# Kernel tuning notes

Measured on AMD Instinct MI355X. Metric: run time of the kernel, lower is better.

The kernel has to match this reference:

```python
import jax, jax.numpy as jnp
import numpy as np

N, F_IN, Z, H, E, ATT, NPER, B = 4096, 512, 256, 256, 64, 128, 16, 128

def setup_inputs() -> dict:
    key = jax.random.key(0)
    ks = jax.random.split(key, 30)
    nrm = lambda k, s, sc=0.05: jax.random.normal(k, s, dtype=jnp.float32) * sc
    return {
        "comm_adj0": jax.random.uniform(ks[0], (N, N), dtype=jnp.float32),
        "comm_adj1": jax.random.uniform(ks[1], (N, N), dtype=jnp.float32),
        "diff_adj0": jax.random.uniform(ks[2], (N, N), dtype=jnp.float32),
        "diff_adj1": jax.random.uniform(ks[3], (N, N), dtype=jnp.float32),
        "feats": nrm(ks[4], (N, F_IN), 1.0),
        "W_comm_gnn": nrm(ks[5], (F_IN, H)), "b_comm_gnn": jnp.zeros((H,), jnp.float32),
        "W_diff_gnn": nrm(ks[6], (F_IN, H)), "b_diff_gnn": jnp.zeros((H,), jnp.float32),
        "W_catt1": nrm(ks[7], (H, ATT)), "b_catt1": jnp.zeros((ATT,), jnp.float32), "w_catt2": nrm(ks[8], (ATT, 1)),
        "W_datt1": nrm(ks[9], (H, ATT)), "b_datt1": jnp.zeros((ATT,), jnp.float32), "w_datt2": nrm(ks[10], (ATT, 1)),
        "W_mu_c": nrm(ks[11], (H, E)), "b_mu_c": jnp.zeros((E,), jnp.float32),
        "W_var_c": nrm(ks[12], (H, E)), "b_var_c": jnp.zeros((E,), jnp.float32),
        "W_mu_d": nrm(ks[13], (H, E)), "b_mu_d": jnp.zeros((E,), jnp.float32),
        "W_var_d": nrm(ks[14], (H, E)), "b_var_d": jnp.zeros((E,), jnp.float32),
        "W_z1_gc1": nrm(ks[15], (F_IN, Z)), "b_z1_gc1": jnp.zeros((Z,), jnp.float32),
        "W_z1_gc2": nrm(ks[16], (Z, Z)), "b_z1_gc2": jnp.zeros((Z,), jnp.float32),
        "wb_z1": jax.random.uniform(ks[17], (2, 1), dtype=jnp.float32, maxval=0.1),
        "Wt_comm": nrm(ks[18], (NPER, E)), "Wt_diff": nrm(ks[19], (NPER, E)),
        "W_z2_gc1": nrm(ks[20], (F_IN, Z)), "b_z2_gc1": jnp.zeros((Z,), jnp.float32),
        "W_z2_gc2": nrm(ks[21], (Z, Z)), "b_z2_gc2": jnp.zeros((Z,), jnp.float32),
        "wb_z2": jax.random.uniform(ks[22], (2, 1), dtype=jnp.float32, maxval=0.1),
        "xs": jax.random.randint(ks[23], (B,), 0, N),
    }

def _gcn(x, adj, W, b):
    # DenseGCNConv: set diag to 1 (self loops), sym-normalize with deg clamped to >=1
    n = adj.shape[0]
    eye = jnp.eye(n, dtype=adj.dtype)
    adj = adj * (1.0 - eye) + eye
    d = jnp.maximum(jnp.sum(adj, axis=-1), 1.0) ** -0.5
    adj_n = d[:, None] * adj * d[None, :]
    return adj_n @ (x @ W) + b

def _attention(z, W1, b1, w2):
    # z: [N, K, H] -> [N, H]
    w = jnp.tanh(z @ W1 + b1) @ w2              # [N, K, 1]
    beta = jax.nn.softmax(jnp.mean(w, axis=0), axis=0)  # [K, 1]
    return jnp.sum(beta[None] * z, axis=1)

def _adj_gen(ctx, Wt):
    # ctx: [N, E], Wt: [P, E]; mean over P of cosine-sim maps, then relu-mask
    cf = ctx[None, :, :] * Wt[:, None, :]                     # [P, N, E]
    cn = cf / jnp.maximum(jnp.linalg.norm(cf, axis=-1, keepdims=True), 1e-12)
    att = jnp.einsum('pne,pme->nm', cn, cn) / Wt.shape[0]     # mean over P without [P,N,N]
    return jnp.maximum(att, 0.0)

def reference(comm_adj0, comm_adj1, diff_adj0, diff_adj1, feats,
              W_comm_gnn, b_comm_gnn, W_diff_gnn, b_diff_gnn,
              W_catt1, b_catt1, w_catt2, W_datt1, b_datt1, w_datt2,
              W_mu_c, b_mu_c, W_var_c, b_var_c, W_mu_d, b_mu_d, W_var_d, b_var_d,
              W_z1_gc1, b_z1_gc1, W_z1_gc2, b_z1_gc2, wb_z1,
              Wt_comm, Wt_diff, W_z2_gc1, b_z2_gc1, W_z2_gc2, b_z2_gc2, wb_z2, xs):
    relu = jax.nn.relu
    comm_adjs = [comm_adj0, comm_adj1]
    diff_adjs = [diff_adj0, diff_adj1]
    # --- q_e2_gs_e1 (eval: dropout=id, reparameterize -> mu) ---
    comm_reps = [relu(_gcn(feats, a, W_comm_gnn, b_comm_gnn)) for a in comm_adjs]
    comm_adj_mean = (comm_adj0 + comm_adj1) * 0.5
    diff_reps = [relu(_gcn(feats, a + comm_adj_mean, W_diff_gnn, b_diff_gnn)) for a in diff_adjs]
    comm_agg = _attention(jnp.stack(comm_reps, axis=1), W_catt1, b_catt1, w_catt2)
    diff_agg = _attention(jnp.stack(comm_reps + diff_reps, axis=1), W_datt1, b_datt1, w_datt2)
    mu_c = relu(comm_agg @ W_mu_c + b_mu_c)
    var_c = jax.nn.sigmoid(relu(comm_agg @ W_var_c + b_var_c))
    mu_d = relu(diff_agg @ W_mu_d + b_mu_d)
    var_d = jax.nn.sigmoid(relu(diff_agg @ W_var_d + b_var_d))
    comm_samples, diff_samples = mu_c, mu_d
    # --- p_z1_gs_e1 (mean pooling over adj stacks) ---
    diff_adj_mean = (diff_adj0 + diff_adj1) * 0.5
    tmp = comm_adj_mean * wb_z1[0, 0] + diff_adj_mean * wb_z1[1, 0]
    final_A1 = tmp + tmp.T
    U1 = relu(_gcn(feats, final_A1, W_z1_gc1, b_z1_gc1))
    U2 = relu(_gcn(U1, final_A1, W_z1_gc2, b_z1_gc2))
    z1 = (U1 + U2) * 0.5
    # --- p_z2_e2 ---
    ca = _adj_gen(comm_samples, Wt_comm)
    da = _adj_gen(diff_samples, Wt_diff)
    tmp2 = ca * wb_z2[0, 0] + da * wb_z2[1, 0]
    final_A2 = tmp2 + tmp2.T
    V1 = relu(_gcn(feats, final_A2, W_z2_gc1, b_z2_gc1))
    V2 = relu(_gcn(V1, final_A2, W_z2_gc2, b_z2_gc2))
    z2 = (V1 + V2) * 0.5
    h = jnp.concatenate([z1, z2], axis=1)
    return (h[xs], mu_c, var_c, mu_d, var_d)
```

## Files before the change

kernel.cpp:

```cpp
#include <hip/hip_runtime.h>
#include <math.h>

using f32x4 = __attribute__((ext_vector_type(4))) float;
using bf16x8 = __attribute__((ext_vector_type(8))) short;
#define MFMA16 __builtin_amdgcn_mfma_f32_16x16x32_bf16
static constexpr size_t M1c = 1048576;

__device__ __forceinline__ float wave_reduce_sum(float v) {
#pragma unroll
  for (int off = 32; off > 0; off >>= 1) v += __shfl_down(v, off);
  return v;
}

__device__ __forceinline__ unsigned short f2bf_rne(float x) {
  unsigned int u = __float_as_uint(x);
  unsigned int r = u + 0x7FFFu + ((u >> 16) & 1u);
  return (unsigned short)(r >> 16);
}
__device__ __forceinline__ void split1(float x, unsigned short& h, unsigned short& l) {
  unsigned int u = __float_as_uint(x);
  h = (unsigned short)(u >> 16);
  float rem = x - __uint_as_float(u & 0xFFFF0000u);
  l = f2bf_rne(rem);
}
// ... 59 lines not shown
  int r0 = blockIdx.y * 128;
  const float4* T4 = (const float4*)T;
  float4 a = make_float4(0.f, 0.f, 0.f, 0.f);
  for (int r = r0; r < r0 + 128; ++r) {
    float4 p = T4[(size_t)r * 1024 + c4];
    a.x += p.x; a.y += p.y; a.z += p.z; a.w += p.w;
  }
  atomicAdd(&cs[c4 * 4 + 0], a.x);
  atomicAdd(&cs[c4 * 4 + 1], a.y);
  atomicAdd(&cs[c4 * 4 + 2], a.z);
  atomicAdd(&cs[c4 * 4 + 3], a.w);
}

__global__ __launch_bounds__(256) void k_addTn(const float* __restrict__ T,
                                               const float* __restrict__ dv,
                                               unsigned short* __restrict__ A1h,
                                               unsigned short* __restrict__ A1l) {
  __shared__ float t[64][65];
  int bi = blockIdx.y, bj = blockIdx.x;
  int r = threadIdx.x >> 4;
  int c4 = threadIdx.x & 15;
#pragma unroll
  for (int rr = 0; rr < 4; ++rr) {
    int row = rr * 16 + r;
    float4 v = *(const float4*)(T + (size_t)(bj * 64 + row) * 4096 + bi * 64 + c4 * 4);
    t[row][c4 * 4 + 0] = v.x; t[row][c4 * 4 + 1] = v.y;
    t[row][c4 * 4 + 2] = v.z; t[row][c4 * 4 + 3] = v.w;
  }
  __syncthreads();
#pragma unroll
  for (int rr = 0; rr < 4; ++rr) {
    int ro = rr * 16 + r;
    int rowg = bi * 64 + ro;
    float dr = dv[rowg];
    size_t idx = (size_t)rowg * 4096 + bj * 64 + c4 * 4;
    float4 a = *(const float4*)(T + idx);
    float f0 = (a.x + t[c4 * 4 + 0][ro]) * dr * dv[bj * 64 + c4 * 4 + 0];
    float f1 = (a.y + t[c4 * 4 + 1][ro]) * dr * dv[bj * 64 + c4 * 4 + 1];
    float f2 = (a.z + t[c4 * 4 + 2][ro]) * dr * dv[bj * 64 + c4 * 4 + 2];
    float f3 = (a.w + t[c4 * 4 + 3][ro]) * dr * dv[bj * 64 + c4 * 4 + 3];
    ushort4 hv, lv;
    split1(f0, ((unsigned short*)&hv)[0], ((unsigned short*)&lv)[0]);
    split1(f1, ((unsigned short*)&hv)[1], ((unsigned short*)&lv)[1]);
    split1(f2, ((unsigned short*)&hv)[2], ((unsigned short*)&lv)[2]);
    split1(f3, ((unsigned short*)&hv)[3], ((unsigned short*)&lv)[3]);
    *(ushort4*)(A1h + idx) = hv;
    *(ushort4*)(A1l + idx) = lv;
  }
}

__global__ __launch_bounds__(256) void k_fin(
    const float* __restrict__ rs_c0, const float* __restrict__ rs_c1,
    const float* __restrict__ rs_d0, const float* __restrict__ rs_d1,
    const float* __restrict__ dg_c0, const float* __restrict__ dg_c1,
    const float* __restrict__ dg_d0, const float* __restrict__ dg_d1,
    const float* __restrict__ cs_tmp, const float* __restrict__ wb,
    float* __restrict__ d_c0, float* __restrict__ d_c1,
    float* __restrict__ d_dd0, float* __restrict__ d_dd1, float* __restrict__ d_A1,
    float* __restrict__ gP_dd0, float* __restrict__ gP_dd1, float* __restrict__ gP_A1) {
  int n = blockIdx.x * 256 + threadIdx.x;
  float rc0 = rs_c0[n], rc1 = rs_c1[n], rd0 = rs_d0[n], rd1 = rs_d1[n];
  float gc0 = dg_c0[n], gc1 = dg_c1[n], gd0 = dg_d0[n], gd1 = dg_d1[n];
  d_c0[n] = rsqrtf(fmaxf(rc0 - gc0 + 1.f, 1.f));
  d_c1[n] = rsqrtf(fmaxf(rc1 - gc1 + 1.f, 1.f));
  float cmr = 0.5f * (rc0 + rc1), cmg = 0.5f * (gc0 + gc1);
  float g0 = gd0 + cmg; gP_dd0[n] = g0;
  d_dd0[n] = rsqrtf(fmaxf(rd0 + cmr - g0 + 1.f, 1.f));
  float g1 = gd1 + cmg; gP_dd1[n] = g1;
  d_dd1[n] = rsqrtf(fmaxf(rd1 + cmr - g1 + 1.f, 1.f));
  float w0 = wb[0], w1 = wb[1];
  float rt = w0 * cmr + w1 * 0.5f * (rd0 + rd1);
  float gt = w0 * cmg + w1 * 0.5f * (gd0 + gd1);
  gP_A1[n] = 2.f * gt;
  d_A1[n] = rsqrtf(fmaxf(rt + cs_tmp[n] - 2.f * gt + 1.f, 1.f));
}

__global__ __launch_bounds__(256) void k_dA2(const float* __restrict__ rs,
                                             const float* __restrict__ gP,
                                             float* __restrict__ dvec) {
  int n = blockIdx.x * 256 + threadIdx.x;
  dvec[n] = rsqrtf(fmaxf(rs[n] - gP[n] + 1.f, 1.f));
}

__global__ __launch_bounds__(256) void k_cn(const float* __restrict__ mu,
                                            const float* __restrict__ Wt,
                                            unsigned short* __restrict__ Chh,
                                            unsigned short* __restrict__ Cll) {
  int g = blockIdx.x * 4 + (threadIdx.x >> 6);
  int lane = threadIdx.x & 63;
  int n = g >> 4, p = g & 15;
  float v = mu[(size_t)n * 64 + lane] * Wt[p * 64 + lane];
  float ss = v * v;
#pragma unroll
  for (int off = 32; off > 0; off >>= 1) ss += __shfl_xor(ss, off);
  float nrm = fmaxf(sqrtf(ss), 1e-12f);
  float r = v / nrm;
  unsigned short h, l;
  split1(r, h, l);
  size_t o = (size_t)n * 1024 + p * 64 + lane;
  Chh[o] = h; Cll[o] = l;
}

__global__ __launch_bounds__(256) void k_prepB(const float* __restrict__ X,
                                               const float* __restrict__ scale,
                                               unsigned short* __restrict__ Bh,
                                               unsigned short* __restrict__ Bl,
                                               int K, int C) {
  __shared__ float t[64][65];
  int kb = blockIdx.x * 64, cb = blockIdx.y * 64;
  int lane = threadIdx.x & 63, w = threadIdx.x >> 6;
  for (int i = 0; i < 16; ++i) {
    int kk = w * 16 + i;
    float s = scale ? scale[kb + kk] : 1.f;
    t[kk][lane] = X[(size_t)(kb + kk) * C + cb + lane] * s;
  }
  __syncthreads();
  for (int i = 0; i < 16; ++i) {
    int cc = w * 16 + i;
    float v = t[lane][cc];
    unsigned short h, l;
    split1(v, h, l);
    size_t o = (size_t)(cb + cc) * K + kb + lane;
    Bh[o] = h; Bl[o] = l;
  }
}

__global__ __launch_bounds__(256) void k_prop4S(
    const float* __restrict__ As0, const float* __restrict__ As1,
    const float* __restrict__ As2, const float* __restrict__ As3,
    const float* __restrict__ Ax0, const float* __restrict__ Ax1, int cmask,
    const float* __restrict__ dsc0, const float* __restrict__ dsc1,
    const float* __restrict__ dsc2, const float* __restrict__ dsc3,
    const unsigned short* __restrict__ B0h, const unsigned short* __restrict__ B0l,
    const unsigned short* __restrict__ B1h, const unsigned short* __restrict__ B1l,
    const unsigned short* __restrict__ B2h, const unsigned short* __restrict__ B2l,
    const unsigned short* __restrict__ B3h, const unsigned short* __restrict__ B3l,
    float* __restrict__ part, int K, int Kc, int KS) {
  int d = blockIdx.x;
  int q = gridDim.x >> 3;
  int lin = (d & 7) * q + (d >> 3);
  int mblk = lin & 63;
  int sk = lin >> 6;
  int seg = sk / KS, kb = sk % KS;
  const float* A = seg == 0 ? As0 : seg == 1 ? As1 : seg == 2 ? As2 : As3;
  const unsigned short* Bh = seg == 0 ? B0h : seg == 1 ? B1h : seg == 2 ? B2h : B3h;
  const unsigned short* Bl = seg == 0 ? B0l : seg == 1 ? B1l : seg == 2 ? B2l : B3l;
  const float* dsc = seg == 0 ? dsc0 : seg == 1 ? dsc1 : seg == 2 ? dsc2 : dsc3;
  const bool usecm = (cmask >> seg) & 1;
  const bool usesc = dsc != nullptr;
  __shared__ unsigned char sm[2][2][8192];
  const int tid = threadIdx.x;
  const int m0 = mblk * 64, k0 = kb * Kc;
  const int w = tid >> 6, lane = tid & 63;
  const int lr = lane & 15, lk = (lane >> 4) * 8, n0w = w * 64;
  const int srow = tid >> 2, skp = (tid & 3) * 8;
  const int swz = (srow & 7) << 4;
  const int offh = (srow * 128 + skp * 2) ^ swz;
  const int offl = (srow * 128 + 64 + skp * 2) ^ swz;
  const size_t rowoff = (size_t)(m0 + srow) * K + k0 + skp;
  const float* arow = A + rowoff;
  const float* xrow0 = Ax0 + rowoff;
  const float* xrow1 = Ax1 + rowoff;
  const float* scrow = usesc ? (dsc + k0 + skp) : nullptr;

  float4 xa0, xa1, xb0, xb1;
  float4 ya0, ya1, yb0, yb1;
  float4 za0, za1, zb0, zb1;
  float4 sa0, sa1, sb0, sb1;
  auto ldPair = [&](int kk) {
    xa0 = *(const float4*)(arow + kk);
    xa1 = *(const float4*)(arow + kk + 4);
    xb0 = *(const float4*)(arow + kk + 32);
    xb1 = *(const float4*)(arow + kk + 36);
    if (usecm) {
      ya0 = *(const float4*)(xrow0 + kk);
      ya1 = *(const float4*)(xrow0 + kk + 4);
      yb0 = *(const float4*)(xrow0 + kk + 32);
      yb1 = *(const float4*)(xrow0 + kk + 36);
      za0 = *(const float4*)(xrow1 + kk);
      za1 = *(const float4*)(xrow1 + kk + 4);
      zb0 = *(const float4*)(xrow1 + kk + 32);
      zb1 = *(const float4*)(xrow1 + kk + 36);
    }
// ... 32 lines not shown
      }
      if (usesc) {
        f[0] *= sb0.x; f[1] *= sb0.y; f[2] *= sb0.z; f[3] *= sb0.w;
        f[4] *= sb1.x; f[5] *= sb1.y; f[6] *= sb1.z; f[7] *= sb1.w;
      }
      bf16x8 hh, ll;
      split8(f, hh, ll);
      *(bf16x8*)(&sm[pb][1][0] + offh) = hh;
      *(bf16x8*)(&sm[pb][1][0] + offl) = ll;
    }
  };

  f32x4 acc[4][4] = {};
  auto comp = [&](int pb, int half, int kkg) {
    const unsigned char* base = &sm[pb][half][0];
    bf16x8 ah[4], al[4];
#pragma unroll
    for (int i = 0; i < 4; ++i) {
      int row = i * 16 + lr, sz = (row & 7) << 4;
      ah[i] = *(const bf16x8*)(base + ((row * 128 + lk * 2) ^ sz));
      al[i] = *(const bf16x8*)(base + ((row * 128 + 64 + lk * 2) ^ sz));
    }
#pragma unroll
    for (int j = 0; j < 4; ++j) {
      int col = n0w + j * 16 + lr;
      size_t bo = (size_t)col * K + kkg;
      bf16x8 bh = *(const bf16x8*)(Bh + bo);
      bf16x8 bl = *(const bf16x8*)(Bl + bo);
#pragma unroll
      for (int i = 0; i < 4; ++i) {
        acc[i][j] = MFMA16(ah[i], bh, acc[i][j], 0, 0, 0);
        acc[i][j] = MFMA16(ah[i], bl, acc[i][j], 0, 0, 0);
        acc[i][j] = MFMA16(al[i], bh, acc[i][j], 0, 0, 0);
      }
    }
  };

  int pairs = Kc / 64;
  ldPair(0);
  wrPair(0);
  __syncthreads();
  for (int p = 0; p < pairs; ++p) {
    if (p + 1 < pairs) ldPair((p + 1) * 64);
    comp(p & 1, 0, k0 + p * 64 + lk);
    comp(p & 1, 1, k0 + p * 64 + 32 + lk);
    if (p + 1 < pairs) wrPair((p + 1) & 1);
    __syncthreads();
  }
  int rr = (lane >> 4) * 4;
  float* Cp = part + (size_t)(seg * KS + kb) * M1c;
#pragma unroll
  for (int i = 0; i < 4; ++i)
#pragma unroll
    for (int j = 0; j < 4; ++j) {
      int col = n0w + j * 16 + lr;
#pragma unroll
      for (int r = 0; r < 4; ++r)
        Cp[(size_t)(m0 + i * 16 + rr + r) * 256 + col] = acc[i][j][r];
    }
}

__global__ __launch_bounds__(256) void k_gemmS(
    const unsigned short* __restrict__ Ah, const unsigned short* __restrict__ Al,
    const unsigned short* __restrict__ Bth, const unsigned short* __restrict__ Btl,
    float* __restrict__ part, int K, int Kc) {
  int d = blockIdx.x;
  int q = gridDim.x >> 3;
  int lin = (d & 7) * q + (d >> 3);
  int mblk = lin & 63;
  int kb = lin >> 6;
  __shared__ unsigned char sm[2][2][8192];
  const int tid = threadIdx.x;
  const int m0 = mblk * 64, k0 = kb * Kc;
  const int w = tid >> 6, lane = tid & 63;
  const int lr = lane & 15, lk = (lane >> 4) * 8, n0w = w * 64;
  const int srow = tid >> 2, skp = (tid & 3) * 8;
  const int swz = (srow & 7) << 4;
  const int offh = (srow * 128 + skp * 2) ^ swz;
  const int offl = (srow * 128 + 64 + skp * 2) ^ swz;
  const unsigned short* arh = Ah + (size_t)(m0 + srow) * K + k0 + skp;
  const unsigned short* arl = Al + (size_t)(m0 + srow) * K + k0 + skp;

  bf16x8 rha, rla, rhb, rlb;
  auto ldPair = [&](int kk) {
    rha = *(const bf16x8*)(arh + kk);
    rla = *(const bf16x8*)(arl + kk);
    rhb = *(const bf16x8*)(arh + kk + 32);
    rlb = *(const bf16x8*)(arl + kk + 32);
  };
  auto wrPair = [&](int pb) {
    *(bf16x8*)(&sm[pb][0][0] + offh) = rha;
    *(bf16x8*)(&sm[pb][0][0] + offl) = rla;
    *(bf16x8*)(&sm[pb][1][0] + offh) = rhb;
    *(bf16x8*)(&sm[pb][1][0] + offl) = rlb;
  };

  f32x4 acc[4][4] = {};
  auto comp = [&](int pb, int half, int kkg) {
    const unsigned char* base = &sm[pb][half][0];
    bf16x8 ah[4], al[4];
#pragma unroll
    for (int i = 0; i < 4; ++i) {
      int row = i * 16 + lr, sz = (row & 7) << 4;
      ah[i] = *(const bf16x8*)(base + ((row * 128 + lk * 2) ^ sz));
      al[i] = *(const bf16x8*)(base + ((row * 128 + 64 + lk * 2) ^ sz));
    }
#pragma unroll
    for (int j = 0; j < 4; ++j) {
      int col = n0w + j * 16 + lr;
      size_t bo = (size_t)col * K + kkg;
      bf16x8 bh = *(const bf16x8*)(Bth + bo);
      bf16x8 bl = *(const bf16x8*)(Btl + bo);
#pragma unroll
      for (int i = 0; i < 4; ++i) {
        acc[i][j] = MFMA16(ah[i], bh, acc[i][j], 0, 0, 0);
        acc[i][j] = MFMA16(ah[i], bl, acc[i][j], 0, 0, 0);
        acc[i][j] = MFMA16(al[i], bh, acc[i][j], 0, 0, 0);
      }
    }
  };

  int pairs = Kc / 64;
  ldPair(0);
  wrPair(0);
  __syncthreads();
  for (int p = 0; p < pairs; ++p) {
    if (p + 1 < pairs) ldPair((p + 1) * 64);
    comp(p & 1, 0, k0 + p * 64 + lk);
    comp(p & 1, 1, k0 + p * 64 + 32 + lk);
    if (p + 1 < pairs) wrPair((p + 1) & 1);
    __syncthreads();
  }
  int rr = (lane >> 4) * 4;
  float* Cp = part + (size_t)kb * M1c;
#pragma unroll
  for (int i = 0; i < 4; ++i)
#pragma unroll
    for (int j = 0; j < 4; ++j) {
      int col = n0w + j * 16 + lr;
#pragma unroll
      for (int r = 0; r < 4; ++r)
        Cp[(size_t)(m0 + i * 16 + rr + r) * 256 + col] = acc[i][j][r];
    }
}

__global__ __launch_bounds__(256) void k_gemmH(
    const float* __restrict__ Aa, const float* __restrict__ Ab,
    const unsigned short* __restrict__ Bth, const unsigned short* __restrict__ Btl,
    float* __restrict__ part, int K, int Kc) {
  __shared__ unsigned char sm[2][2][8192];
  const int tid = threadIdx.x;
  const int m0 = blockIdx.y * 64, k0 = blockIdx.x * Kc;
  const int w = tid >> 6, lane = tid & 63;
  const int lr = lane & 15, lk = (lane >> 4) * 8, n0w = w * 64;
  const int srow = tid >> 2, skp = (tid & 3) * 8;
  const int swz = (srow & 7) << 4;
  const int offh = (srow * 128 + skp * 2) ^ swz;
  const int offl = (srow * 128 + 64 + skp * 2) ^ swz;
  const int slot = w >> 1;

  auto stage = [&](int b, int kk) {
    int kg = k0 + kk + skp;
    const float* p = Aa + (size_t)(m0 + srow) * K + kg;
    float4 x0 = *(const float4*)(p), x1 = *(const float4*)(p + 4);
    float f[8] = {x0.x, x0.y, x0.z, x0.w, x1.x, x1.y, x1.z, x1.w};
    bf16x8 hh, ll;
    split8(f, hh, ll);
    *(bf16x8*)(&sm[b][0][0] + offh) = hh;
    *(bf16x8*)(&sm[b][0][0] + offl) = ll;
    const float* qq = Ab + (size_t)(m0 + srow) * K + kg;
    float4 y0 = *(const float4*)(qq), y1 = *(const float4*)(qq + 4);
    float g[8] = {y0.x, y0.y, y0.z, y0.w, y1.x, y1.y, y1.z, y1.w};
    split8(g, hh, ll);
    *(bf16x8*)(&sm[b][1][0] + offh) = hh;
    *(bf16x8*)(&sm[b][1][0] + offl) = ll;
  };

  f32x4 acc[4][4] = {};
  stage(0, 0);
  __syncthreads();
  int steps = Kc / 32;
  for (int s = 0; s < steps; ++s) {
    if (s + 1 < steps) stage((s + 1) & 1, (s + 1) * 32);
    const unsigned char* base = &sm[s & 1][slot][0];
    bf16x8 ah[4], al[4];
#pragma unroll
    for (int i = 0; i < 4; ++i) {
      int row = i * 16 + lr, sz = (row & 7) << 4;
      ah[i] = *(const bf16x8*)(base + ((row * 128 + lk * 2) ^ sz));
      al[i] = *(const bf16x8*)(base + ((row * 128 + 64 + lk * 2) ^ sz));
    }
    int kkg = k0 + s * 32 + lk;
#pragma unroll
    for (int j = 0; j < 4; ++j) {
      int col = n0w + j * 16 + lr;
      size_t bo = (size_t)col * K + kkg;
      bf16x8 bh = *(const bf16x8*)(Bth + bo);
      bf16x8 bl = *(const bf16x8*)(Btl + bo);
#pragma unroll
      for (int i = 0; i < 4; ++i) {
        acc[i][j] = MFMA16(ah[i], bh, acc[i][j], 0, 0, 0);
        acc[i][j] = MFMA16(ah[i], bl, acc[i][j], 0, 0, 0);
        acc[i][j] = MFMA16(al[i], bh, acc[i][j], 0, 0, 0);
      }
    }
    __syncthreads();
  }
  int rr = (lane >> 4) * 4;
  float* Cp = part + (size_t)blockIdx.x * M1c;
#pragma unroll
  for (int i = 0; i < 4; ++i)
#pragma unroll
    for (int j = 0; j < 4; ++j) {
// ... 146 lines not shown
        int sz = (rowb & 7) << 4;
        bf16x8 bh = *(const bf16x8*)(bb + ((rowb * 128 + lk * 2) ^ sz));
        bf16x8 bl = *(const bf16x8*)(bb + ((rowb * 128 + 64 + lk * 2) ^ sz));
#pragma unroll
        for (int i = 0; i < 4; ++i) {
          acc[i][j] = MFMA16(ah[i], bh, acc[i][j], 0, 0, 0);
          acc[i][j] = MFMA16(ah[i], bl, acc[i][j], 0, 0, 0);
          acc[i][j] = MFMA16(al[i], bh, acc[i][j], 0, 0, 0);
        }
      }
      if (s + 1 < 32) {
        wrT((s + 1) & 1, 0, rA);
        wrT((s + 1) & 1, 1, rB);
      }
      __syncthreads();
    }
  };

  f32x4 aC[4][4] = {}, aD[4][4] = {};
  gram(Ch, Cl, aC);
  gram(Dh, Dl, aD);

  float w0 = wb[0] * 0.125f, w1 = wb[1] * 0.125f;
  int rr = (lane >> 4) * 4;
  bool diag = (bi == bj);
#pragma unroll
  for (int i = 0; i < 4; ++i) {
#pragma unroll
    for (int r = 0; r < 4; ++r) {
      int row = rbase + wm * 64 + i * 16 + rr + r;
      float p = 0.f;
#pragma unroll
      for (int j = 0; j < 4; ++j) {
        int col = cbase + wn * 64 + j * 16 + lr;
        float v = w0 * fmaxf(aC[i][j][r], 0.f) + w1 * fmaxf(aD[i][j][r], 0.f);
        p += v;
        unsigned short h, l;
        split1(v, h, l);
        size_t o = (size_t)row * 4096 + col;
        A2h[o] = h; A2l[o] = l;
        if (diag && row == col) gP[row] = v;
      }
      p += __shfl_xor(p, 1); p += __shfl_xor(p, 2);
      p += __shfl_xor(p, 4); p += __shfl_xor(p, 8);
      if (lr == 0) atomicAdd(&rs[row], p);
    }
  }
  if (!diag) {
#pragma unroll
    for (int j = 0; j < 4; ++j) {
      int col = cbase + wn * 64 + j * 16 + lr;
      float cs = 0.f;
#pragma unroll
      for (int i = 0; i < 4; ++i) {
        int row0m = rbase + wm * 64 + i * 16 + rr;
        ushort4 hv, lv;
#pragma unroll
        for (int r = 0; r < 4; ++r) {
          float v = w0 * fmaxf(aC[i][j][r], 0.f) + w1 * fmaxf(aD[i][j][r], 0.f);
          cs += v;
          unsigned short h, l;
          split1(v, h, l);
          ((unsigned short*)&hv)[r] = h;
          ((unsigned short*)&lv)[r] = l;
        }
        *(ushort4*)(A2h + (size_t)col * 4096 + row0m) = hv;
        *(ushort4*)(A2l + (size_t)col * 4096 + row0m) = lv;
      }
      cs += __shfl_xor(cs, 16); cs += __shfl_xor(cs, 32);
      if (lane < 16) atomicAdd(&rs[col], cs);
    }
  }
}

__global__ __launch_bounds__(256) void k_redxw(
    const float* __restrict__ part, float* __restrict__ o0, float* __restrict__ o1,
    float* __restrict__ o2, float* __restrict__ o3) {
  int idx = blockIdx.x * 256 + threadIdx.x;
  size_t i4 = (size_t)idx * 4;
  int seg = (int)(i4 >> 20);
  size_t local = i4 & (M1c - 1);
  float4 a = make_float4(0.f, 0.f, 0.f, 0.f);
#pragma unroll
  for (int kb = 0; kb < 4; ++kb) {
    float4 p = *(const float4*)(part + (size_t)(seg * 4 + kb) * M1c + local);
    a.x += p.x; a.y += p.y; a.z += p.z; a.w += p.w;
  }
  float* o = seg == 0 ? o0 : seg == 1 ? o1 : seg == 2 ? o2 : o3;
  *(float4*)(o + local) = a;
}

__global__ __launch_bounds__(256) void k_ep_prop4(
    const float* __restrict__ part, const float* __restrict__ xwc,
    const float* __restrict__ xwd, const float* __restrict__ dv0,
    const float* __restrict__ dv1, const float* __restrict__ dv2,
    const float* __restrict__ dv3, const float* __restrict__ dg0,
    const float* __restrict__ dg1, const float* __restrict__ dg2,
    const float* __restrict__ dg3, const float* __restrict__ bc,
    const float* __restrict__ bd, float* __restrict__ o0, float* __restrict__ o1,
    float* __restrict__ o2, float* __restrict__ o3) {
  int idx = blockIdx.x * 256 + threadIdx.x;
  size_t i4 = (size_t)idx * 4;
  int seg = (int)(i4 >> 20);
  size_t local = i4 & (M1c - 1);
  int row = (int)(local >> 8), c = (int)(local & 255);
  float4 a = make_float4(0.f, 0.f, 0.f, 0.f);
#pragma unroll
  for (int kb = 0; kb < 2; ++kb) {
    float4 p = *(const float4*)(part + (size_t)(seg * 2 + kb) * M1c + local);
    a.x += p.x; a.y += p.y; a.z += p.z; a.w += p.w;
  }
  const float* xw = (seg < 2) ? xwc : xwd;
  const float* dvec = seg == 0 ? dv0 : seg == 1 ? dv1 : seg == 2 ? dv2 : dv3;
  const float* dgp = seg == 0 ? dg0 : seg == 1 ? dg1 : seg == 2 ? dg2 : dg3;
  const float* bias = (seg < 2) ? bc : bd;
  float* out = seg == 0 ? o0 : seg == 1 ? o1 : seg == 2 ? o2 : o3;
  float4 x = *(const float4*)(xw + local);
  float4 b = *(const float4*)(bias + c);
  float dn = dvec[row], dfix = (1.f - dgp[row]) * dn * dn;
  float4 o;
  o.x = fmaxf(dn * a.x + dfix * x.x + b.x, 0.f);
  o.y = fmaxf(dn * a.y + dfix * x.y + b.y, 0.f);
  o.z = fmaxf(dn * a.z + dfix * x.z + b.z, 0.f);
  o.w = fmaxf(dn * a.w + dfix * x.w + b.w, 0.f);
  *(float4*)(out + local) = o;
}

template <int PRENORM, int SPLITOUT>
__global__ __launch_bounds__(256) void k_ep_prop(
    const float* __restrict__ part, const float* __restrict__ xw,
    const float* __restrict__ dvec, const float* __restrict__ diag,
    const float* __restrict__ bias, float* __restrict__ out,
    unsigned short* __restrict__ oh, unsigned short* __restrict__ ol) {
  int idx = blockIdx.x * 256 + threadIdx.x;
  size_t i = (size_t)idx * 4;
  int row = (int)(i >> 8), c = (int)(i & 255);
  float4 a = make_float4(0.f, 0.f, 0.f, 0.f);
#pragma unroll
  for (int kb = 0; kb < 8; ++kb) {
    float4 p = *(const float4*)(part + (size_t)kb * M1c + i);
    a.x += p.x; a.y += p.y; a.z += p.z; a.w += p.w;
  }
  float4 x = *(const float4*)(xw + i);
  float4 b = *(const float4*)(bias + c);
  float dn = dvec[row], dfix = (1.f - diag[row]) * dn * dn;
  float s = PRENORM ? 1.f : dn;
  float4 o;
  o.x = fmaxf(s * a.x + dfix * x.x + b.x, 0.f);
  o.y = fmaxf(s * a.y + dfix * x.y + b.y, 0.f);
  o.z = fmaxf(s * a.z + dfix * x.z + b.z, 0.f);
  o.w = fmaxf(s * a.w + dfix * x.w + b.w, 0.f);
  *(float4*)(out + i) = o;
  if constexpr (SPLITOUT) {
    ushort4 hv, lv;
    split1(o.x, ((unsigned short*)&hv)[0], ((unsigned short*)&lv)[0]);
    split1(o.y, ((unsigned short*)&hv)[1], ((unsigned short*)&lv)[1]);
    split1(o.z, ((unsigned short*)&hv)[2], ((unsigned short*)&lv)[2]);
    split1(o.w, ((unsigned short*)&hv)[3], ((unsigned short*)&lv)[3]);
    *(ushort4*)(oh + i) = hv;
    *(ushort4*)(ol + i) = lv;
  }
}

__global__ __launch_bounds__(256) void k_red2(const float* __restrict__ part,
                                              float* __restrict__ out) {
  int idx = blockIdx.x * 256 + threadIdx.x;
  size_t i = (size_t)idx * 4;
  float4 p0 = *(const float4*)(part + i);
// ... 110 lines not shown
  const float* b_z1_2 = (const float*)d_in[26];
  const float* wb_z1 = (const float*)d_in[27];
  const float* Wt_c = (const float*)d_in[28];
  const float* Wt_d = (const float*)d_in[29];
  const float* W_z2_1 = (const float*)d_in[30];
  const float* b_z2_1 = (const float*)d_in[31];
  const float* W_z2_2 = (const float*)d_in[32];
  const float* b_z2_2 = (const float*)d_in[33];
  const float* wb_z2 = (const float*)d_in[34];
  const int* xs = (const int*)d_in[35];

  float* out = (float*)d_out;
  float* out_muc = out + 65536;
  float* out_varc = out + 327680;
  float* out_mud = out + 589824;
  float* out_vard = out + 851968;

  float* ws = (float*)d_ws;
  const size_t M1 = M1c;
  float* xw_comm = ws + 0 * M1;
  float* xw_diff = ws + 1 * M1;
  float* xw_z1 = ws + 2 * M1;
  float* xw_z2 = ws + 3 * M1;
  float* cr0 = ws + 4 * M1;
  float* cr1 = ws + 5 * M1;
  float* dr0 = ws + 6 * M1;
  float* dr1 = ws + 7 * M1;
  float* u1 = ws + 8 * M1;
  float* u2 = ws + 9 * M1;
  float* v1 = ws + 10 * M1;
  float* v2 = ws + 11 * M1;
  float* uw = ws + 12 * M1;
  float* cagg = ws + 13 * M1;
  float* dagg = ws + 14 * M1;
  float* accb4 = ws + 15 * M1;
  unsigned short* B4h[4];
  unsigned short* B4l[4];
  for (int t = 0; t < 4; ++t) {
    B4h[t] = (unsigned short*)(ws + (19 + t) * M1);
    B4l[t] = B4h[t] + (size_t)256 * 4096;
  }
  unsigned short* A1h = (unsigned short*)(ws + 23 * M1);
  unsigned short* A1l = (unsigned short*)(ws + 31 * M1);
  unsigned short* Cch = (unsigned short*)(ws + 23 * M1);
  unsigned short* Ccl = (unsigned short*)(ws + 25 * M1);
  unsigned short* Cdh = (unsigned short*)(ws + 27 * M1);
  unsigned short* Cdl = (unsigned short*)(ws + 29 * M1);
  float* partZ2 = ws + 31 * M1;
  float* tmpb = ws + 39 * M1;
  float* part16 = ws + 39 * M1;
  float* partZ1 = ws + 39 * M1;
  unsigned short* A2h = (unsigned short*)(ws + 39 * M1);
  unsigned short* A2l = (unsigned short*)(ws + 47 * M1);
  unsigned short* u1h = (unsigned short*)(ws + 55 * M1);
  unsigned short* u1l = u1h + (size_t)4096 * 256;
  unsigned short* v1h = (unsigned short*)(ws + 56 * M1);
  unsigned short* v1l = v1h + (size_t)4096 * 256;
  float* vecs = ws + 57 * M1;
#define VV(i) (vecs + (size_t)(i) * 4096)
  float* rs_c0 = VV(0); float* rs_c1 = VV(1); float* rs_d0 = VV(2); float* rs_d1 = VV(3);
  float* dg_c0 = VV(4); float* dg_c1 = VV(5); float* dg_d0 = VV(6); float* dg_d1 = VV(7);
  float* cs_tmp = VV(8); float* rs_A2 = VV(9);
  float* d_c0 = VV(10); float* d_c1 = VV(11); float* d_dd0 = VV(12); float* d_dd1 = VV(13);
  float* d_A1 = VV(14); float* d_A2 = VV(15);
  float* gP_dd0 = VV(16); float* gP_dd1 = VV(17); float* gP_A1 = VV(18); float* gP_A2 = VV(19);
  float* satt = VV(20);
  float* beta = satt + 8;

  hipMemsetAsync(cs_tmp, 0, 2 * 4096 * sizeof(float), stream);
  hipMemsetAsync(satt, 0, 64, stream);

  k_rowsums<<<256, 256, 0, stream>>>(c0adj, c1adj, d0adj, d1adj, wb_z1, tmpb,
                                     rs_c0, rs_c1, rs_d0, rs_d1, dg_c0, dg_c1, dg_d0, dg_d1);
  k_colsum<<<dim3(4, 32), 256, 0, stream>>>(tmpb, cs_tmp);
  k_fin<<<16, 256, 0, stream>>>(rs_c0, rs_c1, rs_d0, rs_d1, dg_c0, dg_c1, dg_d0, dg_d1,
                                cs_tmp, wb_z1, d_c0, d_c1, d_dd0, d_dd1, d_A1,
                                gP_dd0, gP_dd1, gP_A1);
  k_addTn<<<dim3(64, 64), 256, 0, stream>>>(tmpb, d_A1, A1h, A1l);

  k_prepB<<<dim3(8, 4), 256, 0, stream>>>(W_comm, nullptr, B4h[0], B4l[0], 512, 256);
  k_prepB<<<dim3(8, 4), 256, 0, stream>>>(W_diff, nullptr, B4h[1], B4l[1], 512, 256);
  k_prepB<<<dim3(8, 4), 256, 0, stream>>>(W_z1_1, nullptr, B4h[2], B4l[2], 512, 256);
  k_prepB<<<dim3(8, 4), 256, 0, stream>>>(W_z2_1, nullptr, B4h[3], B4l[3], 512, 256);
  k_prop4S<<<1024, 256, 0, stream>>>(
      feats, feats, feats, feats, feats, feats, 0,
      nullptr, nullptr, nullptr, nullptr,
      B4h[0], B4l[0], B4h[1], B4l[1], B4h[2], B4l[2], B4h[3], B4l[3],
      part16, 512, 128, 4);
  k_redxw<<<4096, 256, 0, stream>>>(part16, xw_comm, xw_diff, xw_z1, xw_z2);

  k_prepB<<<dim3(64, 4), 256, 0, stream>>>(xw_comm, nullptr, B4h[0], B4l[0], 4096, 256);
  k_prepB<<<dim3(64, 4), 256, 0, stream>>>(xw_diff, nullptr, B4h[1], B4l[1], 4096, 256);
  k_prop4S<<<512, 256, 0, stream>>>(
      c0adj, c1adj, d0adj, d1adj, c0adj, c1adj, 0xC,
      d_c0, d_c1, d_dd0, d_dd1,
      B4h[0], B4l[0], B4h[0], B4l[0], B4h[1], B4l[1], B4h[1], B4l[1],
      part16, 4096, 2048, 2);
  k_ep_prop4<<<4096, 256, 0, stream>>>(part16, xw_comm, xw_diff, d_c0, d_c1, d_dd0, d_dd1,
                                       dg_c0, dg_c1, gP_dd0, gP_dd1, b_comm, b_diff,
                                       cr0, cr1, dr0, dr1);

  unsigned short* Bth = B4h[0];
  unsigned short* BtlL = Bth + (size_t)256 * 4096;
  unsigned short* BthS = Bth;
  unsigned short* BtlS = Bth + (size_t)256 * 256;

  k_prepB<<<dim3(64, 4), 256, 0, stream>>>(xw_z1, nullptr, Bth, BtlL, 4096, 256);
  k_gemmS<<<512, 256, 0, stream>>>(A1h, A1l, Bth, BtlL, partZ1, 4096, 512);
  k_ep_prop<1, 1><<<1024, 256, 0, stream>>>(partZ1, xw_z1, d_A1, gP_A1, b_z1_1, u1, u1h, u1l);
  k_prepB<<<dim3(4, 4), 256, 0, stream>>>(W_z1_2, nullptr, BthS, BtlS, 256, 256);
  k_gemmS<<<128, 256, 0, stream>>>(u1h, u1l, BthS, BtlS, accb4, 256, 128);
  k_red2<<<1024, 256, 0, stream>>>(accb4, uw);
  k_prepB<<<dim3(64, 4), 256, 0, stream>>>(uw, nullptr, Bth, BtlL, 4096, 256);
  k_gemmS<<<512, 256, 0, stream>>>(A1h, A1l, Bth, BtlL, partZ1, 4096, 512);
  k_ep_prop<1, 0><<<1024, 256, 0, stream>>>(partZ1, uw, d_A1, gP_A1, b_z1_2, u2, nullptr, nullptr);

  {
    unsigned short* Wch = B4h[1];
    unsigned short* Wcl = Wch + (size_t)128 * 256;
    unsigned short* Wdh = B4h[2];
    unsigned short* Wdl = Wdh + (size_t)128 * 256;
    k_prepB<<<dim3(4, 2), 256, 0, stream>>>(W_catt1, nullptr, Wch, Wcl, 256, 128);
    k_prepB<<<dim3(4, 2), 256, 0, stream>>>(W_datt1, nullptr, Wdh, Wdl, 256, 128);
    k_attG<<<dim3(64, 6), 256, 0, stream>>>(cr0, cr1, dr0, dr1, Wch, Wcl, Wdh, Wdl,
                                            b_catt1, w_catt2, b_datt1, w_datt2, satt);
  }
  k_beta<<<1, 64, 0, stream>>>(satt, beta);
  k_agg<<<1024, 256, 0, stream>>>(cr0, cr1, dr0, dr1, beta, cagg, dagg);

  {
    unsigned short* Hh = B4h[0];
    unsigned short* Hl = Hh + (size_t)256 * 256;
    k_prepB<<<dim3(4, 1), 256, 0, stream>>>(W_mu_c, nullptr, Hh + 0 * 64 * 256, Hl + 0 * 64 * 256, 256, 64);
    k_prepB<<<dim3(4, 1), 256, 0, stream>>>(W_var_c, nullptr, Hh + 1 * 64 * 256, Hl + 1 * 64 * 256, 256, 64);
    k_prepB<<<dim3(4, 1), 256, 0, stream>>>(W_mu_d, nullptr, Hh + 2 * 64 * 256, Hl + 2 * 64 * 256, 256, 64);
    k_prepB<<<dim3(4, 1), 256, 0, stream>>>(W_var_d, nullptr, Hh + 3 * 64 * 256, Hl + 3 * 64 * 256, 256, 64);
    k_gemmH<<<dim3(4, 64), 256, 0, stream>>>(cagg, dagg, Hh, Hl, accb4, 256, 64);
    k_ep_heads<<<1024, 256, 0, stream>>>(accb4, b_mu_c, b_var_c, b_mu_d, b_var_d,
                                         out_muc, out_varc, out_mud, out_vard);
  }

  k_cn<<<16384, 256, 0, stream>>>(out_muc, Wt_c, Cch, Ccl);
  k_cn<<<16384, 256, 0, stream>>>(out_mud, Wt_d, Cdh, Cdl);

  k_cos2<<<528, 256, 0, stream>>>(Cch, Ccl, Cdh, Cdl, wb_z2, rs_A2, gP_A2, A2h, A2l);
  k_dA2<<<16, 256, 0, stream>>>(rs_A2, gP_A2, d_A2);

  k_prepB<<<dim3(64, 4), 256, 0, stream>>>(xw_z2, d_A2, Bth, BtlL, 4096, 256);
  k_gemmS<<<512, 256, 0, stream>>>(A2h, A2l, Bth, BtlL, partZ2, 4096, 512);
  k_ep_prop<0, 1><<<1024, 256, 0, stream>>>(partZ2, xw_z2, d_A2, gP_A2, b_z2_1, v1, v1h, v1l);
  k_prepB<<<dim3(4, 4), 256, 0, stream>>>(W_z2_2, nullptr, BthS, BtlS, 256, 256);
  k_gemmS<<<128, 256, 0, stream>>>(v1h, v1l, BthS, BtlS, accb4, 256, 128);
  k_red2<<<1024, 256, 0, stream>>>(accb4, uw);
  k_prepB<<<dim3(64, 4), 256, 0, stream>>>(uw, d_A2, Bth, BtlL, 4096, 256);
  k_gemmS<<<512, 256, 0, stream>>>(A2h, A2l, Bth, BtlL, partZ2, 4096, 512);
  k_ep_prop<0, 0><<<1024, 256, 0, stream>>>(partZ2, uw, d_A2, gP_A2, b_z2_2, v2, nullptr, nullptr);

  k_gather<<<128, 256, 0, stream>>>(xs, u1, u2, v1, v2, out);
}
```

Measured before the change: 1.030 ms.

## Deepen gemmS A-tile prefetch, halve feats split-K, and fuse cosine-normalize launches

The split-K GEMM kernel now prefetches A tiles two iterations ahead, using two alternating register sets, to hide more global-load latency. The first feature projection is split into 2 K-chunks of 256 instead of 4 of 128, so the reduction kernel reads fewer partial buffers. The two cosine-normalisation launches are merged into one kernel that selects its inputs by block index. The gains come from better latency hiding and less launch and reduction traffic, paid for with more registers in gemmS and less grid parallelism in the feats projection.

New measurement: 1.009 ms. 2.0% less time.

```diff
diff --git a/kernel.cpp b/kernel.cpp
--- a/kernel.cpp
+++ b/kernel.cpp
@@ -165,13 +165,20 @@
   dvec[n] = rsqrtf(fmaxf(rs[n] - gP[n] + 1.f, 1.f));
 }
 
-__global__ __launch_bounds__(256) void k_cn(const float* __restrict__ mu,
-                                            const float* __restrict__ Wt,
-                                            unsigned short* __restrict__ Chh,
-                                            unsigned short* __restrict__ Cll) {
+__global__ __launch_bounds__(256) void k_cn2(
+    const float* __restrict__ mu_c, const float* __restrict__ Wt_c,
+    const float* __restrict__ mu_d, const float* __restrict__ Wt_d,
+    unsigned short* __restrict__ Cch, unsigned short* __restrict__ Ccl,
+    unsigned short* __restrict__ Cdh, unsigned short* __restrict__ Cdl) {
   int g = blockIdx.x * 4 + (threadIdx.x >> 6);
   int lane = threadIdx.x & 63;
-  int n = g >> 4, p = g & 15;
+  bool dsel = g >= 65536;
+  int gg = dsel ? g - 65536 : g;
+  const float* mu = dsel ? mu_d : mu_c;
+  const float* Wt = dsel ? Wt_d : Wt_c;
+  unsigned short* Oh = dsel ? Cdh : Cch;
+  unsigned short* Ol = dsel ? Cdl : Ccl;
+  int n = gg >> 4, p = gg & 15;
   float v = mu[(size_t)n * 64 + lane] * Wt[p * 64 + lane];
   float ss = v * v;
 #pragma unroll
@@ -181,7 +188,7 @@
   unsigned short h, l;
   split1(r, h, l);
   size_t o = (size_t)n * 1024 + p * 64 + lane;
-  Chh[o] = h; Cll[o] = l;
+  Oh[o] = h; Ol[o] = l;
 }
 
 __global__ __launch_bounds__(256) void k_prepB(const float* __restrict__ X,
@@ -380,17 +387,30 @@
   const unsigned short* arl = Al + (size_t)(m0 + srow) * K + k0 + skp;
 
   bf16x8 rha, rla, rhb, rlb;
-  auto ldPair = [&](int kk) {
+  bf16x8 sha, sla, shb, slb;
+  auto ld0 = [&](int kk) {
     rha = *(const bf16x8*)(arh + kk);
     rla = *(const bf16x8*)(arl + kk);
     rhb = *(const bf16x8*)(arh + kk + 32);
     rlb = *(const bf16x8*)(arl + kk + 32);
   };
-  auto wrPair = [&](int pb) {
+  auto ld1 = [&](int kk) {
+    sha = *(const bf16x8*)(arh + kk);
+    sla = *(const bf16x8*)(arl + kk);
+    shb = *(const bf16x8*)(arh + kk + 32);
+    slb = *(const bf16x8*)(arl + kk + 32);
+  };
+  auto wr0 = [&](int pb) {
     *(bf16x8*)(&sm[pb][0][0] + offh) = rha;
     *(bf16x8*)(&sm[pb][0][0] + offl) = rla;
     *(bf16x8*)(&sm[pb][1][0] + offh) = rhb;
     *(bf16x8*)(&sm[pb][1][0] + offl) = rlb;
+  };
+  auto wr1 = [&](int pb) {
+    *(bf16x8*)(&sm[pb][0][0] + offh) = sha;
+    *(bf16x8*)(&sm[pb][0][0] + offl) = sla;
+    *(bf16x8*)(&sm[pb][1][0] + offh) = shb;
+    *(bf16x8*)(&sm[pb][1][0] + offl) = slb;
   };
 
   f32x4 acc[4][4] = {};
@@ -419,14 +439,19 @@
   };
 
   int pairs = Kc / 64;
-  ldPair(0);
-  wrPair(0);
+  ld0(0);
+  wr0(0);
+  if (pairs > 1) ld1(64);
   __syncthreads();
   for (int p = 0; p < pairs; ++p) {
-    if (p + 1 < pairs) ldPair((p + 1) * 64);
+    if (p + 2 < pairs) {
+      if ((p & 1) == 0) ld0((p + 2) * 64); else ld1((p + 2) * 64);
+    }
     comp(p & 1, 0, k0 + p * 64 + lk);
     comp(p & 1, 1, k0 + p * 64 + 32 + lk);
-    if (p + 1 < pairs) wrPair((p + 1) & 1);
+    if (p + 1 < pairs) {
+      if (((p + 1) & 1) == 0) wr0((p + 1) & 1); else wr1((p + 1) & 1);
+    }
     __syncthreads();
   }
   int rr = (lane >> 4) * 4;
@@ -739,8 +764,8 @@
   size_t local = i4 & (M1c - 1);
   float4 a = make_float4(0.f, 0.f, 0.f, 0.f);
 #pragma unroll
-  for (int kb = 0; kb < 4; ++kb) {
-    float4 p = *(const float4*)(part + (size_t)(seg * 4 + kb) * M1c + local);
+  for (int kb = 0; kb < 2; ++kb) {
+    float4 p = *(const float4*)(part + (size_t)(seg * 2 + kb) * M1c + local);
     a.x += p.x; a.y += p.y; a.z += p.z; a.w += p.w;
   }
   float* o = seg == 0 ? o0 : seg == 1 ? o1 : seg == 2 ? o2 : o3;
@@ -1017,11 +1042,11 @@
   k_prepB<<<dim3(8, 4), 256, 0, stream>>>(W_diff, nullptr, B4h[1], B4l[1], 512, 256);
   k_prepB<<<dim3(8, 4), 256, 0, stream>>>(W_z1_1, nullptr, B4h[2], B4l[2], 512, 256);
   k_prepB<<<dim3(8, 4), 256, 0, stream>>>(W_z2_1, nullptr, B4h[3], B4l[3], 512, 256);
-  k_prop4S<<<1024, 256, 0, stream>>>(
+  k_prop4S<<<512, 256, 0, stream>>>(
       feats, feats, feats, feats, feats, feats, 0,
       nullptr, nullptr, nullptr, nullptr,
       B4h[0], B4l[0], B4h[1], B4l[1], B4h[2], B4l[2], B4h[3], B4l[3],
-      part16, 512, 128, 4);
+      part16, 512, 256, 2);
   k_redxw<<<4096, 256, 0, stream>>>(part16, xw_comm, xw_diff, xw_z1, xw_z2);
 
   k_prepB<<<dim3(64, 4), 256, 0, stream>>>(xw_comm, nullptr, B4h[0], B4l[0], 4096, 256);
@@ -1075,8 +1100,7 @@
                                          out_muc, out_varc, out_mud, out_vard);
   }
 
-  k_cn<<<16384, 256, 0, stream>>>(out_muc, Wt_c, Cch, Ccl);
-  k_cn<<<16384, 256, 0, stream>>>(out_mud, Wt_d, Cdh, Cdl);
+  k_cn2<<<32768, 256, 0, stream>>>(out_muc, Wt_c, out_mud, Wt_d, Cch, Ccl, Cdh, Cdl);
 
   k_cos2<<<528, 256, 0, stream>>>(Cch, Ccl, Cdh, Cdl, wb_z2, rs_A2, gP_A2, A2h, A2l);
   k_dA2<<<16, 256, 0, stream>>>(rs_A2, gP_A2, d_A2);
```
